# Optimization experiments

Measured on AMD Instinct MI355X. Metric: run time of the kernel, lower is better.

## Reference

```python
import jax, jax.numpy as jnp
import numpy as np

DIVISOR = 2.0
NEGATIVE_SLOPE = 0.01


def setup_inputs() -> dict:
    key = jax.random.key(0)
    k1, k2, k3 = jax.random.split(key, 3)
    x = jax.random.normal(k1, (32, 128, 130, 130), dtype=jnp.float32)
    weight = jax.random.normal(k2, (256, 128, 3, 3), dtype=jnp.float32) * 0.05
    bias = jax.random.normal(k3, (256,), dtype=jnp.float32)
    return {"x": x, "weight": weight, "bias": bias}


def reference(x, weight, bias):
    # conv2d, stride=1, padding=0 (VALID), NCHW / OIHW layout
    y = jax.lax.conv_general_dilated(
        x, weight,
        window_strides=(1, 1),
        padding='VALID',
        dimension_numbers=('NCHW', 'OIHW', 'NCHW'),
    )
    y = y + bias[None, :, None, None]
    y = y * (1.0 / DIVISOR)
    # fused LeakyReLU epilogue
    return jnp.where(y >= 0, y, y * NEGATIVE_SLOPE)
```

## Files before the change

### kernel.cpp

```cpp
#include <hip/hip_runtime.h>
#include <hip/hip_bf16.h>
#include <stdint.h>

typedef __bf16 bf16x8 __attribute__((ext_vector_type(8)));
typedef float  f32x4  __attribute__((ext_vector_type(4)));

#define NSLOPE 0.01f

#define NB   32
#define CIN  128
#define HIN  130
#define WIN  130
#define KOUT 256
#define POUT 128
#define QOUT 128
#define HWIN (HIN*WIN)

#define XP_BYTES 138444800ull
#define WP_ELEMS (2*3*3*KOUT*64)

__device__ __forceinline__ unsigned short f2bf(float f) {
    unsigned u = __builtin_bit_cast(unsigned, f);
    u += 0x7FFFu + ((u >> 16) & 1u);
    return (unsigned short)(u >> 16);
}

__device__ __forceinline__ void g2lds16(const void* g, void* l) {
    __builtin_amdgcn_global_load_lds(
        (const __attribute__((address_space(1))) void*)g,
        (__attribute__((address_space(3))) void*)l,
        16, 0, 0);
}

__global__ __launch_bounds__(256) void k_conv_x(const float* __restrict__ X,
                                                unsigned short* __restrict__ Xp) {
    __shared__ unsigned short tile[130*132];
    const int b = blockIdx.x;
    const int n = b / 130, h = b - n*130;
    const int tid = threadIdx.x;
    const size_t in_base = (size_t)n*(CIN*(size_t)HWIN) + (size_t)h*WIN;
    for (int fi = tid; fi < CIN*WIN; fi += 256) {
        int c = fi / WIN, w = fi - c*WIN;
        tile[w*132 + c] = f2bf(X[in_base + (size_t)c*HWIN + w]);
    }
    __syncthreads();
    unsigned short* outp = Xp + (size_t)b * (WIN*CIN);
    for (int oi = tid; oi < (WIN*CIN)/4; oi += 256) {
        int e = oi*4; int w = e >> 7; int c4 = e & 127;
        const unsigned short* t = &tile[w*132 + c4];
        ushort4 v; v.x = t[0]; v.y = t[1]; v.z = t[2]; v.w = t[3];
        *(ushort4*)(outp + e) = v;
    }
}

__global__ __launch_bounds__(256) void k_conv_w(const float* __restrict__ W,
                                                unsigned short* __restrict__ Wp) {
    int e = blockIdx.x*256 + threadIdx.x;
    if (e >= WP_ELEMS) return;
    int ci = e & 63;
    int k  = (e >> 6) & 255;
    int rsIdx = e >> 14;
    int cc = rsIdx / 9; int rem = rsIdx - cc*9; int r = rem / 3, s = rem - r*3;
    int c = cc*64 + ci;
    Wp[e] = f2bf(W[(size_t)k*1152 + (size_t)c*9 + r*3 + s]);
}

#define LDS_WS_OFF 16640
#define LDS_TOTAL  (16640 + 49152)

__global__ __launch_bounds__(256, 2) void k_conv_main(
    const unsigned short* __restrict__ Xp,
    const unsigned short* __restrict__ Wp,
    const float* __restrict__ bias,
    float* __restrict__ out)
{
    __shared__ __align__(16) unsigned char smem[LDS_TOTAL];

    const int tid  = threadIdx.x;
    const int lane = tid & 63;
    const int wid  = tid >> 6;
    const int wm   = wid >> 1;
    const int wn   = wid & 1;
    const int l15  = lane & 15;
    const int kg   = lane >> 4;

    const int L  = ((blockIdx.x & 7) << 10) | (blockIdx.x >> 3);
    const int kh = L & 1;
    const int np = L >> 1;
    const int p  = np & 127;
    const int n  = np >> 7;
    const int k0 = kh << 7;

    f32x4 acc[4][4];
    #pragma unroll
    for (int i = 0; i < 4; ++i)
        #pragma unroll
        for (int j = 0; j < 4; ++j)
            acc[i][j] = (f32x4){0.f, 0.f, 0.f, 0.f};

    for (int cc = 0; cc < 2; ++cc) {
        for (int r = 0; r < 3; ++r) {
            __syncthreads();
            {
                const unsigned short* wbase = Wp + ((size_t)((cc*3 + r)*3)*KOUT + k0)*64;
                #pragma unroll
                for (int it = 0; it < 12; ++it) {
                    const int t    = it*256 + tid;
                    const int phys = t << 4;
                    const int grow = phys >> 7;
                    const int cib  = (phys & 127) ^ ((grow & 7) << 4);
                    const int s    = grow >> 7;
                    const int kk   = grow & 127;
                    const unsigned short* src = wbase + ((size_t)(s*KOUT + kk))*64 + (cib >> 1);
                    g2lds16(src, smem + LDS_WS_OFF + phys);
                }
            }
            {
                const unsigned short* xbase = Xp + ((size_t)(n*HIN + (p + r))*WIN)*CIN + cc*64;
                #pragma unroll
                for (int it = 0; it < 5; ++it) {
                    const int t = it*256 + tid;
                    if (t < 1040) {
                        const int phys = t << 4;
                        const int w    = phys >> 7;
                        const int cib  = (phys & 127) ^ ((w & 7) << 4);
                        const unsigned short* src = xbase + (size_t)w*CIN + (cib >> 1);
                        g2lds16(src, smem + phys);
                    }
                }
            }
            asm volatile("s_waitcnt vmcnt(0)" ::: "memory");
            __syncthreads();

            #pragma unroll
            for (int s = 0; s < 3; ++s) {
                #pragma unroll
                for (int kq = 0; kq < 2; ++kq) {
                    const int cib = kq*64 + kg*16;
                    bf16x8 af[4], bx[4];
                    #pragma unroll
                    for (int mf = 0; mf < 4; ++mf) {
                        const int row = wm*64 + mf*16 + l15;
                        af[mf] = *(const bf16x8*)(smem + LDS_WS_OFF + s*16384 + row*128
                                                  + (cib ^ ((row & 7) << 4)));
                    }
                    #pragma unroll
                    for (int nf = 0; nf < 4; ++nf) {
                        const int w = wn*64 + nf*16 + l15 + s;
                        bx[nf] = *(const bf16x8*)(smem + w*128 + (cib ^ ((w & 7) << 4)));
                    }
                    #pragma unroll
                    for (int mf = 0; mf < 4; ++mf)
                        #pragma unroll
                        for (int nf = 0; nf < 4; ++nf)
                            acc[mf][nf] = __builtin_amdgcn_mfma_f32_16x16x32_bf16(
                                af[mf], bx[nf], acc[mf][nf], 0, 0, 0);
                }
            }
        }
    }

    #pragma unroll
    for (int mf = 0; mf < 4; ++mf) {
        const int kb = k0 + wm*64 + mf*16 + kg*4;
        const float4 bv = *(const float4*)(bias + kb);
        const float bj[4] = {bv.x, bv.y, bv.z, bv.w};
        #pragma unroll
        for (int nf = 0; nf < 4; ++nf) {
            const int q = wn*64 + nf*16 + l15;
            const size_t base = (((size_t)n*KOUT + kb)*POUT + p)*QOUT + q;
            #pragma unroll
            for (int j = 0; j < 4; ++j) {
                float y = (acc[mf][nf][j] + bj[j]) * 0.5f;
                out[base + (size_t)j*(POUT*QOUT)] = (y >= 0.f) ? y : y*NSLOPE;
            }
        }
    }
}

extern "C" void kernel_launch(void* const* d_in, const int* in_sizes, int n_in,
                              void* d_out, int out_size, void* d_ws, size_t ws_size,
                              hipStream_t stream) {
    const float* X = (const float*)d_in[0];
    const float* W = (const float*)d_in[1];
    const float* B = (const float*)d_in[2];
    float* out = (float*)d_out;
    unsigned short* Xp = (unsigned short*)d_ws;
    unsigned short* Wp = (unsigned short*)((char*)d_ws + XP_BYTES);

    k_conv_x   <<<NB*HIN, 256, 0, stream>>>(X, Xp);
    k_conv_w   <<<(WP_ELEMS + 255)/256, 256, 0, stream>>>(W, Wp);
    k_conv_main<<<8192,    256, 0, stream>>>(Xp, Wp, B, out);
}
```

Measured before the change: 436.6 us.

## Double-buffer LDS and enlarge conv tile to all channels across two rows

The main conv kernel now uses 512-thread blocks, each computing all 256 output channels for two output rows. Before, a block covered 128 channels of one row. Weight slices (per filter tap) and input rows (per filter row) are double-buffered in dynamic LDS, about 129 KB. The next stage's global-to-LDS copies are issued before the current MFMA work, with raised wave priority around the MFMA block. This aims to hide load latency behind compute and to cut redundant weight and input traffic per output. In exchange it needs a large LDS footprint, so only one block fits per CU, and it adds extra barriers per step.

```diff
diff --git a/kernel.cpp b/kernel.cpp
--- a/kernel.cpp
+++ b/kernel.cpp
@@ -18,6 +18,11 @@
 
 #define XP_BYTES 138444800ull
 #define WP_ELEMS (2*3*3*KOUT*64)
+
+#define WS_BYTES 32768
+#define XS_BYTES 33280
+#define XS_BASE  65536
+#define LDS_TOTAL 132096
 
 __device__ __forceinline__ unsigned short f2bf(float f) {
     unsigned u = __builtin_bit_cast(unsigned, f);
@@ -65,110 +70,128 @@
     Wp[e] = f2bf(W[(size_t)k*1152 + (size_t)c*9 + r*3 + s]);
 }
 
-#define LDS_WS_OFF 16640
-#define LDS_TOTAL  (16640 + 49152)
-
-__global__ __launch_bounds__(256, 2) void k_conv_main(
+__device__ __forceinline__ void stage_w_half(const unsigned short* __restrict__ Wp,
+                                             unsigned char* lds, int rsidx, int tid, int half) {
+    const unsigned short* wbase = Wp + (size_t)rsidx * (KOUT*64);
+    #pragma unroll
+    for (int it = half*2; it < half*2 + 2; ++it) {
+        const int t    = it*512 + tid;
+        const int phys = t << 4;
+        const int row  = phys >> 7;
+        const int cib  = (phys & 127) ^ ((row & 7) << 4);
+        g2lds16(wbase + (size_t)row*64 + (cib >> 1), lds + phys);
+    }
+}
+
+__device__ __forceinline__ void stage_x(const unsigned short* __restrict__ Xp,
+                                        unsigned char* lds, int n, int h0, int cc, int tid) {
+    #pragma unroll
+    for (int it = 0; it < 5; ++it) {
+        const int t = it*512 + tid;
+        if (t < 2080) {
+            const int phys = t << 4;
+            const int g    = phys >> 7;
+            const int pl   = (g >= 130) ? 1 : 0;
+            const int w    = g - 130*pl;
+            const int cib  = (phys & 127) ^ ((g & 7) << 4);
+            const unsigned short* src =
+                Xp + ((size_t)((n*HIN + h0 + pl)*WIN + w))*CIN + cc*64 + (cib >> 1);
+            g2lds16(src, lds + phys);
+        }
+    }
+}
+
+__global__ __launch_bounds__(512, 2) void k_conv_main(
     const unsigned short* __restrict__ Xp,
     const unsigned short* __restrict__ Wp,
     const float* __restrict__ bias,
     float* __restrict__ out)
 {
-    __shared__ __align__(16) unsigned char smem[LDS_TOTAL];
+    extern __shared__ __align__(16) unsigned char smem[];
 
     const int tid  = threadIdx.x;
     const int lane = tid & 63;
     const int wid  = tid >> 6;
-    const int wm   = wid >> 1;
-    const int wn   = wid & 1;
+    const int wm   = wid >> 2;
+    const int wn   = wid & 3;
     const int l15  = lane & 15;
     const int kg   = lane >> 4;
 
-    const int L  = ((blockIdx.x & 7) << 10) | (blockIdx.x >> 3);
-    const int kh = L & 1;
-    const int np = L >> 1;
-    const int p  = np & 127;
-    const int n  = np >> 7;
-    const int k0 = kh << 7;
-
-    f32x4 acc[4][4];
-    #pragma unroll
-    for (int i = 0; i < 4; ++i)
+    const int L     = ((blockIdx.x & 7) << 8) | (blockIdx.x >> 3);
+    const int ppair = L & 63;
+    const int n     = L >> 6;
+    const int p2    = ppair << 1;
+
+    f32x4 acc[8][4];
+    #pragma unroll
+    for (int i = 0; i < 8; ++i)
         #pragma unroll
         for (int j = 0; j < 4; ++j)
             acc[i][j] = (f32x4){0.f, 0.f, 0.f, 0.f};
 
-    for (int cc = 0; cc < 2; ++cc) {
-        for (int r = 0; r < 3; ++r) {
-            __syncthreads();
-            {
-                const unsigned short* wbase = Wp + ((size_t)((cc*3 + r)*3)*KOUT + k0)*64;
+    stage_w_half(Wp, smem, 0, tid, 0);
+    stage_w_half(Wp, smem, 0, tid, 1);
+    stage_x(Xp, smem + XS_BASE, n, p2, 0, tid);
+    asm volatile("s_waitcnt vmcnt(0)" ::: "memory");
+    __builtin_amdgcn_s_barrier();
+
+    for (int t = 0; t < 18; ++t) {
+        const int cc  = t / 9;
+        const int rem = t - cc*9;
+        const int s   = rem % 3;
+        unsigned char* wsR = smem + (t & 1)*WS_BYTES;
+        unsigned char* xsR = smem + XS_BASE + (((unsigned)t/3) & 1)*XS_BYTES;
+        const int  tn    = t + 1;
+        const bool haveW = (tn < 18);
+        const bool haveX = haveW && (tn % 3 == 0);
+        unsigned char* wsW = smem + (tn & 1)*WS_BYTES;
+        unsigned char* xsW = smem + XS_BASE + (((unsigned)tn/3) & 1)*XS_BYTES;
+
+        #pragma unroll
+        for (int kq = 0; kq < 2; ++kq) {
+            const int cib0 = kq*64 + kg*16;
+            bf16x8 af[8], bx[4];
+            #pragma unroll
+            for (int mf = 0; mf < 8; ++mf) {
+                const int row = wm*128 + mf*16 + l15;
+                af[mf] = *(const bf16x8*)(wsR + row*128 + (cib0 ^ ((row & 7) << 4)));
+            }
+            #pragma unroll
+            for (int nf = 0; nf < 4; ++nf) {
+                const int qq   = wn*64 + nf*16 + l15;
+                const int row2 = (qq >> 7)*130 + (qq & 127) + s;
+                bx[nf] = *(const bf16x8*)(xsR + row2*128 + (cib0 ^ ((row2 & 7) << 4)));
+            }
+            if (haveW) stage_w_half(Wp, wsW, tn, tid, kq);
+            if (kq == 1 && haveX) stage_x(Xp, xsW, n, p2 + (tn % 9) / 3, tn / 9, tid);
+
+            __builtin_amdgcn_s_barrier();
+            asm volatile("s_waitcnt lgkmcnt(0)" ::: "memory");
+            __builtin_amdgcn_sched_barrier(0);
+            __builtin_amdgcn_s_setprio(1);
+            #pragma unroll
+            for (int mf = 0; mf < 8; ++mf)
                 #pragma unroll
-                for (int it = 0; it < 12; ++it) {
-                    const int t    = it*256 + tid;
-                    const int phys = t << 4;
-                    const int grow = phys >> 7;
-                    const int cib  = (phys & 127) ^ ((grow & 7) << 4);
-                    const int s    = grow >> 7;
-                    const int kk   = grow & 127;
-                    const unsigned short* src = wbase + ((size_t)(s*KOUT + kk))*64 + (cib >> 1);
-                    g2lds16(src, smem + LDS_WS_OFF + phys);
-                }
-            }
-            {
-                const unsigned short* xbase = Xp + ((size_t)(n*HIN + (p + r))*WIN)*CIN + cc*64;
-                #pragma unroll
-                for (int it = 0; it < 5; ++it) {
-                    const int t = it*256 + tid;
-                    if (t < 1040) {
-                        const int phys = t << 4;
-                        const int w    = phys >> 7;
-                        const int cib  = (phys & 127) ^ ((w & 7) << 4);
-                        const unsigned short* src = xbase + (size_t)w*CIN + (cib >> 1);
-                        g2lds16(src, smem + phys);
-                    }
-                }
-            }
-            asm volatile("s_waitcnt vmcnt(0)" ::: "memory");
-            __syncthreads();
-
-            #pragma unroll
-            for (int s = 0; s < 3; ++s) {
-                #pragma unroll
-                for (int kq = 0; kq < 2; ++kq) {
-                    const int cib = kq*64 + kg*16;
-                    bf16x8 af[4], bx[4];
-                    #pragma unroll
-                    for (int mf = 0; mf < 4; ++mf) {
-                        const int row = wm*64 + mf*16 + l15;
-                        af[mf] = *(const bf16x8*)(smem + LDS_WS_OFF + s*16384 + row*128
-                                                  + (cib ^ ((row & 7) << 4)));
-                    }
-                    #pragma unroll
-                    for (int nf = 0; nf < 4; ++nf) {
-                        const int w = wn*64 + nf*16 + l15 + s;
-                        bx[nf] = *(const bf16x8*)(smem + w*128 + (cib ^ ((w & 7) << 4)));
-                    }
-                    #pragma unroll
-                    for (int mf = 0; mf < 4; ++mf)
-                        #pragma unroll
-                        for (int nf = 0; nf < 4; ++nf)
-                            acc[mf][nf] = __builtin_amdgcn_mfma_f32_16x16x32_bf16(
-                                af[mf], bx[nf], acc[mf][nf], 0, 0, 0);
-                }
-            }
+                for (int nf = 0; nf < 4; ++nf)
+                    acc[mf][nf] = __builtin_amdgcn_mfma_f32_16x16x32_bf16(
+                        af[mf], bx[nf], acc[mf][nf], 0, 0, 0);
+            __builtin_amdgcn_s_setprio(0);
+            if (kq == 1)
+                asm volatile("s_waitcnt vmcnt(0)" ::: "memory");
+            __builtin_amdgcn_s_barrier();
         }
     }
 
     #pragma unroll
-    for (int mf = 0; mf < 4; ++mf) {
-        const int kb = k0 + wm*64 + mf*16 + kg*4;
+    for (int mf = 0; mf < 8; ++mf) {
+        const int kb = wm*128 + mf*16 + kg*4;
         const float4 bv = *(const float4*)(bias + kb);
         const float bj[4] = {bv.x, bv.y, bv.z, bv.w};
         #pragma unroll
         for (int nf = 0; nf < 4; ++nf) {
-            const int q = wn*64 + nf*16 + l15;
-            const size_t base = (((size_t)n*KOUT + kb)*POUT + p)*QOUT + q;
+            const int qq = wn*64 + nf*16 + l15;
+            const int pl = qq >> 7, q = qq & 127;
+            const size_t base = (((size_t)n*KOUT + kb)*POUT + (p2 + pl))*QOUT + q;
             #pragma unroll
             for (int j = 0; j < 4; ++j) {
                 float y = (acc[mf][nf][j] + bj[j]) * 0.5f;
@@ -188,7 +211,10 @@
     unsigned short* Xp = (unsigned short*)d_ws;
     unsigned short* Wp = (unsigned short*)((char*)d_ws + XP_BYTES);
 
+    (void)hipFuncSetAttribute((const void*)k_conv_main,
+                              hipFuncAttributeMaxDynamicSharedMemorySize, LDS_TOTAL);
+
     k_conv_x   <<<NB*HIN, 256, 0, stream>>>(X, Xp);
     k_conv_w   <<<(WP_ELEMS + 255)/256, 256, 0, stream>>>(W, Wp);
-    k_conv_main<<<8192,    256, 0, stream>>>(Xp, Wp, B, out);
-}
+    k_conv_main<<<2048, 512, LDS_TOTAL, stream>>>(Xp, Wp, B, out);
+}
```

Measured after the change: 445.6 us. 2.1% more time.

## Stream weight fragments from global into registers and stage 4 input rows in LDS

Applied to the files above, without the earlier changes.

The weights are pre-packed into a per-lane MFMA fragment layout so each wave loads its A operands straight from global memory into registers, double-buffered across the 3x3 taps. Each block now covers two output rows with a 4x8 MFMA tile per wave, and stages all four needed input rows for 64 channels into LDS once per channel half. This replaces the per-tap weight and input staging and its barriers. The aim is to cut LDS traffic and synchronisation and to raise reuse per block. In exchange it holds more accumulator registers at the same launch bounds, needs 66 KB of dynamic LDS, and relies on the L2 cache to serve the repeated weight loads.

```diff
diff --git a/kernel.cpp b/kernel.cpp
--- a/kernel.cpp
+++ b/kernel.cpp
@@ -15,9 +15,16 @@
 #define POUT 128
 #define QOUT 128
 #define HWIN (HIN*WIN)
+#define PQ   (POUT*QOUT)
 
 #define XP_BYTES 138444800ull
-#define WP_ELEMS (2*3*3*KOUT*64)
+#define WP_ELEMS (18*2*8*2*64*8)
+
+#define XS_BYTES 66560
+
+#define SB0()    __builtin_amdgcn_sched_barrier(0)
+#define VMW(n)   asm volatile("s_waitcnt vmcnt(" #n ")" ::: "memory")
+#define LGKMW(n) asm volatile("s_waitcnt lgkmcnt(" #n ")" ::: "memory")
 
 __device__ __forceinline__ unsigned short f2bf(float f) {
     unsigned u = __builtin_bit_cast(unsigned, f);
@@ -57,24 +64,72 @@
                                                 unsigned short* __restrict__ Wp) {
     int e = blockIdx.x*256 + threadIdx.x;
     if (e >= WP_ELEMS) return;
-    int ci = e & 63;
-    int k  = (e >> 6) & 255;
-    int rsIdx = e >> 14;
-    int cc = rsIdx / 9; int rem = rsIdx - cc*9; int r = rem / 3, s = rem - r*3;
-    int c = cc*64 + ci;
-    Wp[e] = f2bf(W[(size_t)k*1152 + (size_t)c*9 + r*3 + s]);
-}
-
-#define LDS_WS_OFF 16640
-#define LDS_TOTAL  (16640 + 49152)
+    int j     = e & 7;
+    int lane  = (e >> 3) & 63;
+    int kq    = (e >> 9) & 1;
+    int fr    = (e >> 10) & 7;
+    int kh    = (e >> 13) & 1;
+    int rsidx = e >> 14;
+    int cc = rsidx / 9; int rem = rsidx - cc*9; int rr = rem / 3, s = rem - rr*3;
+    int kout = kh*128 + fr*16 + (lane & 15);
+    int ci   = cc*64 + kq*32 + (lane >> 4)*8 + j;
+    Wp[e] = f2bf(W[(size_t)kout*1152 + (size_t)ci*9 + rr*3 + s]);
+}
+
+__device__ __forceinline__ void stage_x4(const unsigned short* __restrict__ Xp,
+                                         unsigned char* lds, int n, int p2, int cc, int tid) {
+    #pragma unroll
+    for (int it = 0; it < 17; ++it) {
+        const int t = it*256 + tid;
+        if (t < 4160) {
+            const int phys = t << 4;
+            const int g    = phys >> 7;
+            const int rloc = g / 130;
+            const int w    = g - 130*rloc;
+            const int cib  = (phys & 127) ^ ((g & 7) << 4);
+            const unsigned short* src =
+                Xp + ((size_t)((n*HIN + p2 + rloc)*WIN + w))*CIN + cc*64 + (cib >> 1);
+            g2lds16(src, lds + phys);
+        }
+    }
+}
+
+#define ISSUE_A(A_, rsidx, kq) do {                                               \
+    const unsigned char* ab_ = wfp + (size_t)(rsidx)*32768 + khOff + wmOff        \
+                               + (kq)*1024 + laneB;                               \
+    A_[0] = *(const bf16x8*)(ab_);                                                \
+    A_[1] = *(const bf16x8*)(ab_ + 2048);                                         \
+    A_[2] = *(const bf16x8*)(ab_ + 4096);                                         \
+    A_[3] = *(const bf16x8*)(ab_ + 6144);                                         \
+} while (0)
+
+#define ISSUE_B(B_, stv, kq) do {                                                 \
+    const int rr_ = (stv) / 3, ss_ = (stv) - rr_*3;                               \
+    const int g0_ = (wn + rr_)*130 + l15 + ss_;                                   \
+    const int gb_ = g0_*128 + (((kq)*64 + kg16) ^ ((g0_ & 7) << 4));              \
+    _Pragma("unroll")                                                             \
+    for (int nf = 0; nf < 8; ++nf)                                                \
+        B_[nf] = *(const bf16x8*)(xs + gb_ + nf*2048);                            \
+} while (0)
+
+#define MMA(A_, B_) do {                                                          \
+    __builtin_amdgcn_s_setprio(1);                                                \
+    _Pragma("unroll")                                                             \
+    for (int mf = 0; mf < 4; ++mf)                                                \
+        _Pragma("unroll")                                                         \
+        for (int nf = 0; nf < 8; ++nf)                                            \
+            acc[mf][nf] = __builtin_amdgcn_mfma_f32_16x16x32_bf16(                \
+                A_[mf], B_[nf], acc[mf][nf], 0, 0, 0);                            \
+    __builtin_amdgcn_s_setprio(0);                                                \
+} while (0)
 
 __global__ __launch_bounds__(256, 2) void k_conv_main(
     const unsigned short* __restrict__ Xp,
-    const unsigned short* __restrict__ Wp,
+    const unsigned short* __restrict__ Wpp,
     const float* __restrict__ bias,
     float* __restrict__ out)
 {
-    __shared__ __align__(16) unsigned char smem[LDS_TOTAL];
+    extern __shared__ __align__(16) unsigned char xs[];
 
     const int tid  = threadIdx.x;
     const int lane = tid & 63;
@@ -83,96 +138,73 @@
     const int wn   = wid & 1;
     const int l15  = lane & 15;
     const int kg   = lane >> 4;
-
-    const int L  = ((blockIdx.x & 7) << 10) | (blockIdx.x >> 3);
-    const int kh = L & 1;
-    const int np = L >> 1;
-    const int p  = np & 127;
-    const int n  = np >> 7;
-    const int k0 = kh << 7;
-
-    f32x4 acc[4][4];
+    const int kg16 = kg << 4;
+    const int laneB = lane << 4;
+
+    const int L   = ((blockIdx.x & 7) << 9) | (blockIdx.x >> 3);
+    const int kh  = L & 1;
+    const int pqt = L >> 1;
+    const int n   = pqt >> 6;
+    const int p2  = (pqt & 63) << 1;
+
+    const unsigned char* wfp = (const unsigned char*)Wpp;
+    const int khOff = kh << 14;
+    const int wmOff = wm << 13;
+
+    f32x4 acc[4][8];
     #pragma unroll
     for (int i = 0; i < 4; ++i)
         #pragma unroll
-        for (int j = 0; j < 4; ++j)
+        for (int j = 0; j < 8; ++j)
             acc[i][j] = (f32x4){0.f, 0.f, 0.f, 0.f};
 
+    bf16x8 A0[4], A1[4], B0[8], B1[8];
+
+    stage_x4(Xp, xs, n, p2, 0, tid);
+    VMW(0);
+    __builtin_amdgcn_s_barrier();
+
+    #pragma unroll 1
     for (int cc = 0; cc < 2; ++cc) {
-        for (int r = 0; r < 3; ++r) {
-            __syncthreads();
-            {
-                const unsigned short* wbase = Wp + ((size_t)((cc*3 + r)*3)*KOUT + k0)*64;
-                #pragma unroll
-                for (int it = 0; it < 12; ++it) {
-                    const int t    = it*256 + tid;
-                    const int phys = t << 4;
-                    const int grow = phys >> 7;
-                    const int cib  = (phys & 127) ^ ((grow & 7) << 4);
-                    const int s    = grow >> 7;
-                    const int kk   = grow & 127;
-                    const unsigned short* src = wbase + ((size_t)(s*KOUT + kk))*64 + (cib >> 1);
-                    g2lds16(src, smem + LDS_WS_OFF + phys);
-                }
-            }
-            {
-                const unsigned short* xbase = Xp + ((size_t)(n*HIN + (p + r))*WIN)*CIN + cc*64;
-                #pragma unroll
-                for (int it = 0; it < 5; ++it) {
-                    const int t = it*256 + tid;
-                    if (t < 1040) {
-                        const int phys = t << 4;
-                        const int w    = phys >> 7;
-                        const int cib  = (phys & 127) ^ ((w & 7) << 4);
-                        const unsigned short* src = xbase + (size_t)w*CIN + (cib >> 1);
-                        g2lds16(src, smem + phys);
-                    }
-                }
-            }
-            asm volatile("s_waitcnt vmcnt(0)" ::: "memory");
-            __syncthreads();
-
-            #pragma unroll
-            for (int s = 0; s < 3; ++s) {
-                #pragma unroll
-                for (int kq = 0; kq < 2; ++kq) {
-                    const int cib = kq*64 + kg*16;
-                    bf16x8 af[4], bx[4];
-                    #pragma unroll
-                    for (int mf = 0; mf < 4; ++mf) {
-                        const int row = wm*64 + mf*16 + l15;
-                        af[mf] = *(const bf16x8*)(smem + LDS_WS_OFF + s*16384 + row*128
-                                                  + (cib ^ ((row & 7) << 4)));
-                    }
-                    #pragma unroll
-                    for (int nf = 0; nf < 4; ++nf) {
-                        const int w = wn*64 + nf*16 + l15 + s;
-                        bx[nf] = *(const bf16x8*)(smem + w*128 + (cib ^ ((w & 7) << 4)));
-                    }
-                    #pragma unroll
-                    for (int mf = 0; mf < 4; ++mf)
-                        #pragma unroll
-                        for (int nf = 0; nf < 4; ++nf)
-                            acc[mf][nf] = __builtin_amdgcn_mfma_f32_16x16x32_bf16(
-                                af[mf], bx[nf], acc[mf][nf], 0, 0, 0);
-                }
-            }
+        const int rsb = cc*9;
+
+        ISSUE_A(A0, rsb, 0); ISSUE_B(B0, 0, 0); SB0();
+        ISSUE_A(A1, rsb, 1); ISSUE_B(B1, 0, 1); SB0();
+
+        #pragma unroll 1
+        for (int st = 0; st < 9; ++st) {
+            VMW(4); LGKMW(8); SB0();
+            MMA(A0, B0); SB0();
+            if (st < 8) { ISSUE_A(A0, rsb + st + 1, 0); ISSUE_B(B0, st + 1, 0); }
+            SB0();
+            if (st < 8) { VMW(4); LGKMW(8); } else { VMW(0); LGKMW(0); }
+            SB0();
+            MMA(A1, B1); SB0();
+            if (st < 8) { ISSUE_A(A1, rsb + st + 1, 1); ISSUE_B(B1, st + 1, 1); }
+            SB0();
+        }
+
+        if (cc == 0) {
+            __builtin_amdgcn_s_barrier();
+            stage_x4(Xp, xs, n, p2, 1, tid);
+            VMW(0);
+            __builtin_amdgcn_s_barrier();
         }
     }
 
     #pragma unroll
     for (int mf = 0; mf < 4; ++mf) {
-        const int kb = k0 + wm*64 + mf*16 + kg*4;
+        const int kb = kh*128 + wm*64 + mf*16 + kg*4;
         const float4 bv = *(const float4*)(bias + kb);
         const float bj[4] = {bv.x, bv.y, bv.z, bv.w};
         #pragma unroll
-        for (int nf = 0; nf < 4; ++nf) {
-            const int q = wn*64 + nf*16 + l15;
-            const size_t base = (((size_t)n*KOUT + kb)*POUT + p)*QOUT + q;
+        for (int nf = 0; nf < 8; ++nf) {
+            const int q = nf*16 + l15;
+            const size_t base = (((size_t)n*KOUT + kb)*POUT + (p2 + wn))*QOUT + q;
             #pragma unroll
             for (int j = 0; j < 4; ++j) {
                 float y = (acc[mf][nf][j] + bj[j]) * 0.5f;
-                out[base + (size_t)j*(POUT*QOUT)] = (y >= 0.f) ? y : y*NSLOPE;
+                out[base + (size_t)j*PQ] = (y >= 0.f) ? y : y*NSLOPE;
             }
         }
     }
@@ -188,7 +220,10 @@
     unsigned short* Xp = (unsigned short*)d_ws;
     unsigned short* Wp = (unsigned short*)((char*)d_ws + XP_BYTES);
 
+    (void)hipFuncSetAttribute((const void*)k_conv_main,
+                              hipFuncAttributeMaxDynamicSharedMemorySize, XS_BYTES);
+
     k_conv_x   <<<NB*HIN, 256, 0, stream>>>(X, Xp);
     k_conv_w   <<<(WP_ELEMS + 255)/256, 256, 0, stream>>>(W, Wp);
-    k_conv_main<<<8192,    256, 0, stream>>>(Xp, Wp, B, out);
-}
+    k_conv_main<<<4096, 256, XS_BYTES, stream>>>(Xp, Wp, B, out);
+}
```

After: 491.8 us. 12.7% more time.

## Restructure conv main loop to 2-wave blocks with per-tap weight staging

Applied to the files above, without the earlier changes.

The main conv kernel moves from 4 waves to 2 waves per block, each wave computing a 64x128 tile (4x8 MFMA fragments), so the 128-wide output row is covered by one wave's N dimension. The loop now runs over 18 (cc,r,s) taps, loading only one 16 KB weight slice per tap and reloading the input row only when s==0. This shrinks LDS from about 65 KB to 33 KB per block. It adds a sync pair per tap and doubles accumulator registers per thread, which may limit occupancy. The transpose kernel also gains float2 loads and 16-byte stores.

```diff
diff --git a/kernel.cpp b/kernel.cpp
--- a/kernel.cpp
+++ b/kernel.cpp
@@ -4,6 +4,7 @@
 
 typedef __bf16 bf16x8 __attribute__((ext_vector_type(8)));
 typedef float  f32x4  __attribute__((ext_vector_type(4)));
+typedef unsigned short ushort8v __attribute__((ext_vector_type(8)));
 
 #define NSLOPE 0.01f
 
@@ -15,9 +16,13 @@
 #define POUT 128
 #define QOUT 128
 #define HWIN (HIN*WIN)
+#define PQ   (POUT*QOUT)
 
 #define XP_BYTES 138444800ull
 #define WP_ELEMS (2*3*3*KOUT*64)
+
+#define XT_OFF    16384
+#define LDS_TOTAL (16384 + 16640)
 
 __device__ __forceinline__ unsigned short f2bf(float f) {
     unsigned u = __builtin_bit_cast(unsigned, f);
@@ -39,17 +44,21 @@
     const int n = b / 130, h = b - n*130;
     const int tid = threadIdx.x;
     const size_t in_base = (size_t)n*(CIN*(size_t)HWIN) + (size_t)h*WIN;
-    for (int fi = tid; fi < CIN*WIN; fi += 256) {
-        int c = fi / WIN, w = fi - c*WIN;
-        tile[w*132 + c] = f2bf(X[in_base + (size_t)c*HWIN + w]);
+    for (int fi = tid; fi < CIN*65; fi += 256) {
+        int c = fi / 65, w2 = fi - c*65;
+        float2 v = *(const float2*)(X + in_base + (size_t)c*HWIN + w2*2);
+        tile[(w2*2  )*132 + c] = f2bf(v.x);
+        tile[(w2*2+1)*132 + c] = f2bf(v.y);
     }
     __syncthreads();
     unsigned short* outp = Xp + (size_t)b * (WIN*CIN);
-    for (int oi = tid; oi < (WIN*CIN)/4; oi += 256) {
-        int e = oi*4; int w = e >> 7; int c4 = e & 127;
-        const unsigned short* t = &tile[w*132 + c4];
-        ushort4 v; v.x = t[0]; v.y = t[1]; v.z = t[2]; v.w = t[3];
-        *(ushort4*)(outp + e) = v;
+    for (int oi = tid; oi < (WIN*CIN)/8; oi += 256) {
+        int e = oi*8; int w = e >> 7; int c8 = e & 127;
+        const unsigned short* t = &tile[w*132 + c8];
+        ushort8v v;
+        #pragma unroll
+        for (int j = 0; j < 8; ++j) v[j] = t[j];
+        *(ushort8v*)(outp + e) = v;
     }
 }
 
@@ -65,10 +74,7 @@
     Wp[e] = f2bf(W[(size_t)k*1152 + (size_t)c*9 + r*3 + s]);
 }
 
-#define LDS_WS_OFF 16640
-#define LDS_TOTAL  (16640 + 49152)
-
-__global__ __launch_bounds__(256, 2) void k_conv_main(
+__global__ __launch_bounds__(128, 2) void k_conv_main(
     const unsigned short* __restrict__ Xp,
     const unsigned short* __restrict__ Wp,
     const float* __restrict__ bias,
@@ -78,101 +84,97 @@
 
     const int tid  = threadIdx.x;
     const int lane = tid & 63;
-    const int wid  = tid >> 6;
-    const int wm   = wid >> 1;
-    const int wn   = wid & 1;
+    const int wm   = tid >> 6;
     const int l15  = lane & 15;
-    const int kg   = lane >> 4;
+    const int kg16 = (lane >> 4) << 4;
 
     const int L  = ((blockIdx.x & 7) << 10) | (blockIdx.x >> 3);
     const int kh = L & 1;
     const int np = L >> 1;
     const int p  = np & 127;
     const int n  = np >> 7;
-    const int k0 = kh << 7;
 
-    f32x4 acc[4][4];
+    f32x4 acc[4][8];
     #pragma unroll
     for (int i = 0; i < 4; ++i)
         #pragma unroll
-        for (int j = 0; j < 4; ++j)
+        for (int j = 0; j < 8; ++j)
             acc[i][j] = (f32x4){0.f, 0.f, 0.f, 0.f};
 
-    for (int cc = 0; cc < 2; ++cc) {
-        for (int r = 0; r < 3; ++r) {
-            __syncthreads();
-            {
-                const unsigned short* wbase = Wp + ((size_t)((cc*3 + r)*3)*KOUT + k0)*64;
-                #pragma unroll
-                for (int it = 0; it < 12; ++it) {
-                    const int t    = it*256 + tid;
-                    const int phys = t << 4;
-                    const int grow = phys >> 7;
-                    const int cib  = (phys & 127) ^ ((grow & 7) << 4);
-                    const int s    = grow >> 7;
-                    const int kk   = grow & 127;
-                    const unsigned short* src = wbase + ((size_t)(s*KOUT + kk))*64 + (cib >> 1);
-                    g2lds16(src, smem + LDS_WS_OFF + phys);
-                }
+    #pragma unroll 1
+    for (int t = 0; t < 18; ++t) {
+        const int cc = t / 9;
+        const int rem = t - cc*9;
+        const int r  = rem / 3;
+        const int s  = rem - r*3;
+
+        __syncthreads();
+
+        {
+            const unsigned short* wbase = Wp + (size_t)t*(KOUT*64) + (size_t)(kh*128)*64;
+            #pragma unroll
+            for (int it = 0; it < 8; ++it) {
+                const int g    = it*128 + tid;
+                const int phys = g << 4;
+                const int row  = phys >> 7;
+                const int cib  = (phys & 127) ^ ((row & 7) << 4);
+                g2lds16(wbase + (size_t)row*64 + (cib >> 1), smem + phys);
             }
-            {
-                const unsigned short* xbase = Xp + ((size_t)(n*HIN + (p + r))*WIN)*CIN + cc*64;
-                #pragma unroll
-                for (int it = 0; it < 5; ++it) {
-                    const int t = it*256 + tid;
-                    if (t < 1040) {
-                        const int phys = t << 4;
-                        const int w    = phys >> 7;
-                        const int cib  = (phys & 127) ^ ((w & 7) << 4);
-                        const unsigned short* src = xbase + (size_t)w*CIN + (cib >> 1);
-                        g2lds16(src, smem + phys);
-                    }
-                }
-            }
-            asm volatile("s_waitcnt vmcnt(0)" ::: "memory");
-            __syncthreads();
-
+        }
+        if (s == 0) {
+            const unsigned short* xbase =
+                Xp + ((size_t)((n*HIN + (p + r))*WIN))*CIN + cc*64;
             #pragma unroll
-            for (int s = 0; s < 3; ++s) {
-                #pragma unroll
-                for (int kq = 0; kq < 2; ++kq) {
-                    const int cib = kq*64 + kg*16;
-                    bf16x8 af[4], bx[4];
-                    #pragma unroll
-                    for (int mf = 0; mf < 4; ++mf) {
-                        const int row = wm*64 + mf*16 + l15;
-                        af[mf] = *(const bf16x8*)(smem + LDS_WS_OFF + s*16384 + row*128
-                                                  + (cib ^ ((row & 7) << 4)));
-                    }
-                    #pragma unroll
-                    for (int nf = 0; nf < 4; ++nf) {
-                        const int w = wn*64 + nf*16 + l15 + s;
-                        bx[nf] = *(const bf16x8*)(smem + w*128 + (cib ^ ((w & 7) << 4)));
-                    }
-                    #pragma unroll
-                    for (int mf = 0; mf < 4; ++mf)
-                        #pragma unroll
-                        for (int nf = 0; nf < 4; ++nf)
-                            acc[mf][nf] = __builtin_amdgcn_mfma_f32_16x16x32_bf16(
-                                af[mf], bx[nf], acc[mf][nf], 0, 0, 0);
+            for (int it = 0; it < 9; ++it) {
+                const int g = it*128 + tid;
+                if (g < 1040) {
+                    const int phys = g << 4;
+                    const int w    = phys >> 7;
+                    const int cib  = (phys & 127) ^ ((w & 7) << 4);
+                    g2lds16(xbase + (size_t)w*CIN + (cib >> 1), smem + XT_OFF + phys);
                 }
             }
         }
+
+        __syncthreads();
+
+        #pragma unroll
+        for (int kq = 0; kq < 2; ++kq) {
+            const int cib0 = kq*64 + kg16;
+            bf16x8 A[4], B[8];
+            #pragma unroll
+            for (int mf = 0; mf < 4; ++mf) {
+                const int row = wm*64 + mf*16 + l15;
+                A[mf] = *(const bf16x8*)(smem + row*128 + (cib0 ^ ((row & 7) << 4)));
+            }
+            #pragma unroll
+            for (int nf = 0; nf < 8; ++nf) {
+                const int g = nf*16 + l15 + s;
+                B[nf] = *(const bf16x8*)(smem + XT_OFF + g*128 + (cib0 ^ ((g & 7) << 4)));
+            }
+            #pragma unroll
+            for (int mf = 0; mf < 4; ++mf)
+                #pragma unroll
+                for (int nf = 0; nf < 8; ++nf)
+                    acc[mf][nf] = __builtin_amdgcn_mfma_f32_16x16x32_bf16(
+                        A[mf], B[nf], acc[mf][nf], 0, 0, 0);
+        }
     }
 
+    const int kg = lane >> 4;
     #pragma unroll
     for (int mf = 0; mf < 4; ++mf) {
-        const int kb = k0 + wm*64 + mf*16 + kg*4;
+        const int kb = kh*128 + wm*64 + mf*16 + kg*4;
         const float4 bv = *(const float4*)(bias + kb);
         const float bj[4] = {bv.x, bv.y, bv.z, bv.w};
         #pragma unroll
-        for (int nf = 0; nf < 4; ++nf) {
-            const int q = wn*64 + nf*16 + l15;
+        for (int nf = 0; nf < 8; ++nf) {
+            const int q = nf*16 + l15;
             const size_t base = (((size_t)n*KOUT + kb)*POUT + p)*QOUT + q;
             #pragma unroll
             for (int j = 0; j < 4; ++j) {
                 float y = (acc[mf][nf][j] + bj[j]) * 0.5f;
-                out[base + (size_t)j*(POUT*QOUT)] = (y >= 0.f) ? y : y*NSLOPE;
+                out[base + (size_t)j*PQ] = (y >= 0.f) ? y : y*NSLOPE;
             }
         }
     }
@@ -190,5 +192,5 @@
 
     k_conv_x   <<<NB*HIN, 256, 0, stream>>>(X, Xp);
     k_conv_w   <<<(WP_ELEMS + 255)/256, 256, 0, stream>>>(W, Wp);
-    k_conv_main<<<8192,    256, 0, stream>>>(Xp, Wp, B, out);
+    k_conv_main<<<8192, 128, 0, stream>>>(Xp, Wp, B, out);
 }
```

Measured after the change: 425.7 us. 1.03x faster.
